# Optimization experiments

Measured on AMD Instinct MI355X. Metric: run time of the kernel, lower is better.

Reference implementation:

```python
import jax, jax.numpy as jnp
import numpy as np

EMBED = 256
HEADS = 8
HDIM = 32
FF = 1024
EPS = 1e-6
EVERY = 8        # stock_attn_every
LAST_DENSE = 16  # stock_attn_last_dense
B, N, T = 2, 256, 256


def rmsnorm(x, w):
    return x * jax.lax.rsqrt(jnp.mean(x * x, axis=-1, keepdims=True) + EPS) * w


def mha(x, Wq, Wk, Wv, Wo, mask=None):
    # x: (B, S, D); mask: (B, S) bool key-padding mask (True = keep)
    b, s, _ = x.shape
    q = (x @ Wq).reshape(b, s, HEADS, HDIM)
    k = (x @ Wk).reshape(b, s, HEADS, HDIM)
    v = (x @ Wv).reshape(b, s, HEADS, HDIM)
    scores = jnp.einsum('bqhd,bkhd->bhqk', q, k) * (HDIM ** -0.5)
    if mask is not None:
        scores = jnp.where(mask[:, None, None, :], scores, jnp.asarray(-1e9, scores.dtype))
    attn = jax.nn.softmax(scores, axis=-1)
    out = jnp.einsum('bhqk,bkhd->bqhd', attn, v).reshape(b, s, HEADS * HDIM)
    return out @ Wo


def active_t(t):
    # static index set: sparse strided steps + last dense window
    lds = max(0, t - LAST_DENSE)
    idx = sorted(set(list(range(0, lds, max(1, EVERY))) + list(range(lds, t))))
    return jnp.asarray(idx, dtype=jnp.int32)


def setup_inputs() -> dict:
    key = jax.random.key(0)
    ks = jax.random.split(key, 16)
    p = lambda k, shape: (jax.random.normal(k, shape, dtype=jnp.float32) * 0.02)
    inp = {
        'h': jax.random.normal(ks[0], (B, N, T, EMBED), dtype=jnp.float32),
        'stock_mask': jnp.ones((B, N), dtype=jnp.int32),
        'norm_t_w': jnp.ones((EMBED,), dtype=jnp.float32),
        'norm_s_w': jnp.ones((EMBED,), dtype=jnp.float32),
        'norm_ff_w': jnp.ones((EMBED,), dtype=jnp.float32),
        'Wq_t': p(ks[1], (EMBED, HEADS * HDIM)),
        'Wk_t': p(ks[2], (EMBED, HEADS * HDIM)),
        'Wv_t': p(ks[3], (EMBED, HEADS * HDIM)),
        'Wo_t': p(ks[4], (HEADS * HDIM, EMBED)),
        'Wq_s': p(ks[5], (EMBED, HEADS * HDIM)),
        'Wk_s': p(ks[6], (EMBED, HEADS * HDIM)),
        'Wv_s': p(ks[7], (EMBED, HEADS * HDIM)),
        'Wo_s': p(ks[8], (HEADS * HDIM, EMBED)),
        'W1': p(ks[9], (EMBED, FF)),
        'b1': jnp.zeros((FF,), dtype=jnp.float32),
        'W2': p(ks[10], (FF, EMBED)),
        'b2': jnp.zeros((EMBED,), dtype=jnp.float32),
    }
    return inp


def reference(h, stock_mask, norm_t_w, norm_s_w, norm_ff_w,
              Wq_t, Wk_t, Wv_t, Wo_t, Wq_s, Wk_s, Wv_s, Wo_s,
              W1, b1, W2, b2):
    b, n, t, d = h.shape
    # --- time attention (per stock, dense over T) ---
    h_t = rmsnorm(h.reshape(b * n, t, d), norm_t_w)
    h = h + mha(h_t, Wq_t, Wk_t, Wv_t, Wo_t).reshape(b, n, t, d)
    # --- sparse-T gather -> stock attention -> scatter back ---
    active = active_t(t)
    tp = active.shape[0]
    h_s = h[:, :, active, :].transpose(0, 2, 1, 3).reshape(b * tp, n, d)
    m = jnp.broadcast_to(stock_mask.astype(bool)[:, None, :], (b, tp, n)).reshape(b * tp, n)
    h_s = mha(rmsnorm(h_s, norm_s_w), Wq_s, Wk_s, Wv_s, Wo_s, mask=m)
    h = h.at[:, :, active, :].add(h_s.reshape(b, tp, n, d).transpose(0, 2, 1, 3))
    # --- FFN ---
    x = rmsnorm(h, norm_ff_w)
    return h + (jax.nn.gelu(x @ W1 + b1) @ W2 + b2)
```

## Files before the change

kernel.cpp:

```cpp
#include <hip/hip_runtime.h>
#include <hip/hip_bf16.h>

typedef __attribute__((ext_vector_type(8))) short short8;
typedef __attribute__((ext_vector_type(4))) float f32x4;

#define TP 46

#define SBAR() asm volatile("s_barrier" ::: "memory")
#define VMCNT4() asm volatile("s_waitcnt vmcnt(4)" ::: "memory")
#define VMCNT0() asm volatile("s_waitcnt vmcnt(0)" ::: "memory")

__device__ __forceinline__ unsigned short f2bf(float f) {
  unsigned int u = __float_as_uint(f);
  u = (u + 0x7fff + ((u >> 16) & 1)) >> 16;
  return (unsigned short)u;
}
__device__ __forceinline__ unsigned short f2bf_fast(float f) {
  return (unsigned short)((__float_as_uint(f) + 0x8000u) >> 16);
}
__device__ __forceinline__ float bf2f(short u) {
  return __uint_as_float((unsigned)(unsigned short)u << 16);
}
__device__ __forceinline__ float fast_rcp(float x) {
#if __has_builtin(__builtin_amdgcn_rcpf)
  return __builtin_amdgcn_rcpf(x);
#else
  return 1.0f / x;
#endif
}
__device__ __forceinline__ float fast_rsq(float x) {
#if __has_builtin(__builtin_amdgcn_rsqf)
  return __builtin_amdgcn_rsqf(x);
#else
  return rsqrtf(x);
#endif
}

__device__ __forceinline__ int act_t(int j) { return j < 30 ? (j << 3) : (210 + j); }

__device__ __forceinline__ void load_lds16(const unsigned short* g, unsigned short* lds_base) {
#if __has_builtin(__builtin_amdgcn_global_load_lds)
  __builtin_amdgcn_global_load_lds(
      (const __attribute__((address_space(1))) unsigned int*)(unsigned long long)g,
      (__attribute__((address_space(3))) unsigned int*)(unsigned int)(unsigned long long)lds_base,
      16, 0, 0);
#else
  int lane = threadIdx.x & 63;
  *(short8*)(lds_base + lane * 8) = *(const short8*)g;
#endif
}

__global__ __launch_bounds__(256) void convw_kernel(
    const float* __restrict__ wq_t, const float* __restrict__ wk_t,
    const float* __restrict__ wv_t, const float* __restrict__ wo_t,
    const float* __restrict__ wq_s, const float* __restrict__ wk_s,
    const float* __restrict__ wv_s, const float* __restrict__ wo_s,
    const float* __restrict__ w1, const float* __restrict__ w2,
    unsigned short* __restrict__ pool) {
  int idx = blockIdx.x * 256 + threadIdx.x;
  float v;
  if (idx < 524288) {
    int tile = idx >> 12, local = idx & 4095;
    int ks = local >> 9, q = local & 511;
    int l = q >> 3, e = q & 7;
    int lr = l & 15, lg = l >> 4;
    int ct = tile & 15, grp = tile >> 4;
    const float* s = (grp == 0) ? wq_t : (grp == 1) ? wk_t : (grp == 2) ? wv_t :
                     (grp == 3) ? wo_t : (grp == 4) ? wq_s : (grp == 5) ? wk_s :
                     (grp == 6) ? wv_s : wo_s;
    v = s[(size_t)(ks * 32 + lg * 8 + e) * 256 + ct * 16 + lr];
  } else if (idx < 786432) {
    int local = idx - 524288;
    int e = local & 7, t = local >> 3;
    int lane = t & 63, ks = (t >> 6) & 7, ct = (t >> 9) & 1, fc = t >> 10;
    int lr = lane & 15, lg = lane >> 4;
    v = w1[(size_t)(ks * 32 + lg * 8 + e) * 1024 + fc * 32 + ct * 16 + lr];
  } else {
    int local = idx - 786432;
    int e2 = local & 7, t = local >> 3;
    int lane = t & 63, ct2 = (t >> 6) & 15, fc = t >> 10;
    int lr = lane & 15, lg = lane >> 4;
    v = w2[(size_t)(fc * 32 + lg * 8 + e2) * 256 + ct2 * 16 + lr];
  }
  pool[idx] = f2bf(v);
}

template<int GATHER>
__global__ __launch_bounds__(256) void qkv_kernel(
    const float* __restrict__ src, const float* __restrict__ nw,
    const unsigned short* __restrict__ WF,
    unsigned short* __restrict__ qb, unsigned short* __restrict__ kb,
    unsigned short* __restrict__ vb, int row_base) {
  __shared__ __align__(16) unsigned short Wbuf[2][8192];
  int tid = threadIdx.x, wv = tid >> 6, lane = tid & 63, lr = lane & 15, lg = lane >> 4;
  int row0 = blockIdx.x * 128 + wv * 32;
  short8 afrag[2][8];
  #pragma unroll
  for (int rt = 0; rt < 2; ++rt) {
    int lrow = row0 + rt * 16 + lr;
    const float* rp;
    if (GATHER) {
      int gr = row_base + lrow;
      int b = gr / 11776; int rem = gr - b * 11776;
      int j = rem >> 8, n = rem & 255;
      rp = src + (((size_t)((b << 8) + n) << 8) + act_t(j)) * 256;
    } else {
      rp = src + (size_t)lrow * 256;
    }
    float4 x[16];
    #pragma unroll
    for (int ks = 0; ks < 8; ++ks) {
      x[ks * 2]     = *(const float4*)(rp + ks * 32 + lg * 8);
      x[ks * 2 + 1] = *(const float4*)(rp + ks * 32 + lg * 8 + 4);
    }
    float ss = 0.f;
    #pragma unroll
    for (int i = 0; i < 16; ++i)
      ss += x[i].x * x[i].x + x[i].y * x[i].y + x[i].z * x[i].z + x[i].w * x[i].w;
    ss += __shfl_xor(ss, 16, 64);
    ss += __shfl_xor(ss, 32, 64);
    float sc = fast_rsq(ss * 0.00390625f + 1e-6f);
    #pragma unroll
    for (int ks = 0; ks < 8; ++ks) {
      float4 w0 = *(const float4*)(nw + ks * 32 + lg * 8);
      float4 w1_ = *(const float4*)(nw + ks * 32 + lg * 8 + 4);
      short8 af;
      af[0] = (short)f2bf_fast(x[ks * 2].x * sc * w0.x);
      af[1] = (short)f2bf_fast(x[ks * 2].y * sc * w0.y);
      af[2] = (short)f2bf_fast(x[ks * 2].z * sc * w0.z);
      af[3] = (short)f2bf_fast(x[ks * 2].w * sc * w0.w);
      af[4] = (short)f2bf_fast(x[ks * 2 + 1].x * sc * w1_.x);
      af[5] = (short)f2bf_fast(x[ks * 2 + 1].y * sc * w1_.y);
      af[6] = (short)f2bf_fast(x[ks * 2 + 1].z * sc * w1_.z);
      af[7] = (short)f2bf_fast(x[ks * 2 + 1].w * sc * w1_.w);
      afrag[rt][ks] = af;
    }
  }
  #pragma unroll
  for (int i = 0; i < 4; ++i) {
    int s = wv * 4 + i;
    load_lds16(WF + (size_t)s * 512 + lane * 8, &Wbuf[0][s * 512]);
  }
  f32x4 zero = {0.f, 0.f, 0.f, 0.f};
  for (int r = 0; r < 24; ++r) {
    SBAR();
    if (r < 23) {
      #pragma unroll
      for (int i = 0; i < 4; ++i) {
        int s = wv * 4 + i;
        load_lds16(WF + (size_t)(r + 1) * 8192 + s * 512 + lane * 8,
                   &Wbuf[(r + 1) & 1][s * 512]);
      }
      VMCNT4();
    } else {
      VMCNT0();
    }
    SBAR();
    #pragma unroll
    for (int sub = 0; sub < 2; ++sub) {
      int t = r * 2 + sub;
      const unsigned short* Ws = &Wbuf[r & 1][sub * 4096];
      f32x4 a0 = zero, a1 = zero;
      #pragma unroll
      for (int ks = 0; ks < 8; ++ks) {
        short8 bw = *(const short8*)&Ws[ks * 512 + lane * 8];
        a0 = __builtin_amdgcn_mfma_f32_16x16x32_bf16(bw, afrag[0][ks], a0, 0, 0, 0);
        a1 = __builtin_amdgcn_mfma_f32_16x16x32_bf16(bw, afrag[1][ks], a1, 0, 0, 0);
      }
      int m = t >> 4, ct = t & 15;
      unsigned short* dst = (m == 0) ? qb : (m == 1) ? kb : vb;
      ushort4 p0, p1;
      p0.x = f2bf_fast(a0[0]); p0.y = f2bf_fast(a0[1]);
      p0.z = f2bf_fast(a0[2]); p0.w = f2bf_fast(a0[3]);
      p1.x = f2bf_fast(a1[0]); p1.y = f2bf_fast(a1[1]);
      p1.z = f2bf_fast(a1[2]); p1.w = f2bf_fast(a1[3]);
      *(ushort4*)(dst + (size_t)(row0 + lr) * 256 + ct * 16 + lg * 4) = p0;
      *(ushort4*)(dst + (size_t)(row0 + 16 + lr) * 256 + ct * 16 + lg * 4) = p1;
    }
  }
}

template<int MODE>
__global__ __launch_bounds__(256) void gemm256_kernel(
    const unsigned short* __restrict__ X, const unsigned short* __restrict__ WF,
    const float* __restrict__ resid, float* __restrict__ outf, int row_base) {
  __shared__ __align__(16) unsigned short Wbuf[2][8192];
  int tid = threadIdx.x, wv = tid >> 6, lane = tid & 63, lr = lane & 15, lg = lane >> 4;
  int row0 = blockIdx.x * 128 + wv * 32;
  short8 afrag[2][8];
  size_t rb[2];
  #pragma unroll
  for (int rt = 0; rt < 2; ++rt) {
    int row = row0 + rt * 16 + lr;
    #pragma unroll
    for (int ks = 0; ks < 8; ++ks)
      afrag[rt][ks] = *(const short8*)(X + (size_t)row * 256 + ks * 32 + lg * 8);
    if (MODE == 1) {
      rb[rt] = (size_t)row * 256;
    } else {
      int gr = row_base + row;
      int b = gr / 11776; int rem = gr - b * 11776;
      int j = rem >> 8, n = rem & 255;
      rb[rt] = (((size_t)((b << 8) + n) << 8) + act_t(j)) * 256;
    }
  }
  #pragma unroll
  for (int i = 0; i < 4; ++i) {
    int s = wv * 4 + i;
    load_lds16(WF + (size_t)s * 512 + lane * 8, &Wbuf[0][s * 512]);
  }
  f32x4 zero = {0.f, 0.f, 0.f, 0.f};
  for (int r = 0; r < 8; ++r) {
    __syncthreads();
    if (r < 7) {
      #pragma unroll
      for (int i = 0; i < 4; ++i) {
        int s = wv * 4 + i;
        load_lds16(WF + (size_t)(r + 1) * 8192 + s * 512 + lane * 8,
                   &Wbuf[(r + 1) & 1][s * 512]);
      }
    }
    __syncthreads();
    #pragma unroll
    for (int sub = 0; sub < 2; ++sub) {
      int t = r * 2 + sub;
      const unsigned short* Ws = &Wbuf[r & 1][sub * 4096];
      f32x4 a0 = zero, a1 = zero;
      #pragma unroll
      for (int ks = 0; ks < 8; ++ks) {
        short8 bw = *(const short8*)&Ws[ks * 512 + lane * 8];
        a0 = __builtin_amdgcn_mfma_f32_16x16x32_bf16(bw, afrag[0][ks], a0, 0, 0, 0);
        a1 = __builtin_amdgcn_mfma_f32_16x16x32_bf16(bw, afrag[1][ks], a1, 0, 0, 0);
      }
      int col = t * 16 + lg * 4;
      if (MODE == 1) {
        float4 r0 = *(const float4*)(resid + rb[0] + col);
        float4 r1 = *(const float4*)(resid + rb[1] + col);
        float4 o0, o1;
        o0.x = r0.x + a0[0]; o0.y = r0.y + a0[1]; o0.z = r0.z + a0[2]; o0.w = r0.w + a0[3];
        o1.x = r1.x + a1[0]; o1.y = r1.y + a1[1]; o1.z = r1.z + a1[2]; o1.w = r1.w + a1[3];
        *(float4*)(outf + rb[0] + col) = o0;
        *(float4*)(outf + rb[1] + col) = o1;
      } else {
        float4 c0 = *(const float4*)(outf + rb[0] + col);
        float4 c1 = *(const float4*)(outf + rb[1] + col);
        c0.x += a0[0]; c0.y += a0[1]; c0.z += a0[2]; c0.w += a0[3];
        c1.x += a1[0]; c1.y += a1[1]; c1.z += a1[2]; c1.w += a1[3];
        *(float4*)(outf + rb[0] + col) = c0;
        *(float4*)(outf + rb[1] + col) = c1;
      }
    }
  }
}

template<int MASKED>
__global__ __launch_bounds__(256) void attn_kernel(
    const unsigned short* __restrict__ Q, const unsigned short* __restrict__ K,
    const unsigned short* __restrict__ V, unsigned short* __restrict__ O,
    const int* __restrict__ mask, int seq_base) {
  __shared__ unsigned short Ksh[256][40];
  __shared__ unsigned short Vtsh[32][264];
  __shared__ unsigned short Psh[4][16][264];
  int head = blockIdx.x, seq = blockIdx.y;
  int hc = head * 32;
  size_t sb = (size_t)seq * 65536;
  int tid = threadIdx.x;
  {
    int c = tid & 3, rbase = tid >> 2;
    #pragma unroll
    for (int i = 0; i < 4; ++i) {
      int r = rbase + i * 64;
      *(short8*)&Ksh[r][c * 8] = *(const short8*)(K + sb + (size_t)r * 256 + hc + c * 8);
      short8 vv = *(const short8*)(V + sb + (size_t)r * 256 + hc + c * 8);
      #pragma unroll
      for (int e = 0; e < 8; ++e) Vtsh[c * 8 + e][r] = (unsigned short)vv[e];
    }
  }
  __syncthreads();
  int wv = tid >> 6, lane = tid & 63, lr = lane & 15, lg = lane >> 4;
  const float scale = 0.17677669529663687f;
  int mb = 0;
  if (MASKED) mb = (seq_base + seq) / TP;
  f32x4 zero = {0.f, 0.f, 0.f, 0.f};
  for (int rt = 0; rt < 4; ++rt) {
    int row0 = wv * 64 + rt * 16;
    short8 aq = *(const short8*)(Q + sb + (size_t)(row0 + lr) * 256 + hc + lg * 8);
    f32x4 s[16];
    #pragma unroll
    for (int ct = 0; ct < 16; ++ct) {
      short8 kb = *(const short8*)&Ksh[ct * 16 + lr][lg * 8];
      s[ct] = __builtin_amdgcn_mfma_f32_16x16x32_bf16(kb, aq, zero, 0, 0, 0);
    }
    #pragma unroll
    for (int ct = 0; ct < 16; ++ct) {
      if (MASKED) {
        const int4 m4 = *(const int4*)(mask + mb * 256 + ct * 16 + lg * 4);
        s[ct][0] = m4.x ? s[ct][0] * scale : -1e9f;
        s[ct][1] = m4.y ? s[ct][1] * scale : -1e9f;
        s[ct][2] = m4.z ? s[ct][2] * scale : -1e9f;
        s[ct][3] = m4.w ? s[ct][3] * scale : -1e9f;
      } else {
        #pragma unroll
        for (int r = 0; r < 4; ++r) s[ct][r] *= scale;
      }
    }
    float mx = -3e38f;
    #pragma unroll
    for (int ct = 0; ct < 16; ++ct)
      #pragma unroll
      for (int r = 0; r < 4; ++r) mx = fmaxf(mx, s[ct][r]);
    mx = fmaxf(mx, __shfl_xor(mx, 16, 64));
    mx = fmaxf(mx, __shfl_xor(mx, 32, 64));
    float sum = 0.f;
    #pragma unroll
    for (int ct = 0; ct < 16; ++ct)
      #pragma unroll
      for (int r = 0; r < 4; ++r) {
        float p = __expf(s[ct][r] - mx);
        s[ct][r] = p; sum += p;
      }
    sum += __shfl_xor(sum, 16, 64);
    sum += __shfl_xor(sum, 32, 64);
    float inv = fast_rcp(sum);
    #pragma unroll
    for (int ct = 0; ct < 16; ++ct) {
      ushort4 pk;
      pk.x = f2bf_fast(s[ct][0] * inv); pk.y = f2bf_fast(s[ct][1] * inv);
      pk.z = f2bf_fast(s[ct][2] * inv); pk.w = f2bf_fast(s[ct][3] * inv);
      *(ushort4*)&Psh[wv][lr][ct * 16 + lg * 4] = pk;
    }
    f32x4 o[2] = {zero, zero};
    #pragma unroll
    for (int ks = 0; ks < 8; ++ks) {
      short8 pa = *(const short8*)&Psh[wv][lr][ks * 32 + lg * 8];
      #pragma unroll
      for (int c2 = 0; c2 < 2; ++c2) {
        short8 vbf = *(const short8*)&Vtsh[c2 * 16 + lr][ks * 32 + lg * 8];
        o[c2] = __builtin_amdgcn_mfma_f32_16x16x32_bf16(vbf, pa, o[c2], 0, 0, 0);
      }
    }
    #pragma unroll
    for (int c2 = 0; c2 < 2; ++c2) {
      ushort4 ok;
      ok.x = f2bf_fast(o[c2][0]); ok.y = f2bf_fast(o[c2][1]);
      ok.z = f2bf_fast(o[c2][2]); ok.w = f2bf_fast(o[c2][3]);
      *(ushort4*)(O + sb + (size_t)(row0 + lr) * 256 + hc + c2 * 16 + lg * 4) = ok;
    }
  }
}

__global__ __launch_bounds__(256, 4) void ffn_kernel(
    float* __restrict__ hio, const float* __restrict__ nw,
    const unsigned short* __restrict__ W1F, const unsigned short* __restrict__ W2F,
    const float* __restrict__ b1, const float* __restrict__ b2) {
  __shared__ __align__(16) unsigned short Wbuf[16384];
  __shared__ __align__(16) unsigned short Psh[4][16][36];
  int tid = threadIdx.x;
  int wv = tid >> 6, lane = tid & 63, lr = lane & 15, lg = lane >> 4;
  int wrow = blockIdx.x * 64 + wv * 16;
  const float* rp = hio + (size_t)(wrow + lr) * 256;
  short8 xfrag[8];
  float ss = 0.f;
  #pragma unroll
  for (int ks = 0; ks < 8; ++ks) {
    float4 a = *(const float4*)(rp + ks * 32 + lg * 8);
    float4 b = *(const float4*)(rp + ks * 32 + lg * 8 + 4);
    ss += a.x * a.x + a.y * a.y + a.z * a.z + a.w * a.w;
    ss += b.x * b.x + b.y * b.y + b.z * b.z + b.w * b.w;
    short8 xf;
    xf[0] = (short)f2bf_fast(a.x); xf[1] = (short)f2bf_fast(a.y);
    xf[2] = (short)f2bf_fast(a.z); xf[3] = (short)f2bf_fast(a.w);
    xf[4] = (short)f2bf_fast(b.x); xf[5] = (short)f2bf_fast(b.y);
    xf[6] = (short)f2bf_fast(b.z); xf[7] = (short)f2bf_fast(b.w);
    xfrag[ks] = xf;
  }
  ss += __shfl_xor(ss, 16, 64);
  ss += __shfl_xor(ss, 32, 64);
  float sc = fast_rsq(ss * 0.00390625f + 1e-6f);
  #pragma unroll
  for (int ks = 0; ks < 8; ++ks) {
    float4 wa = *(const float4*)(nw + ks * 32 + lg * 8);
    float4 wb = *(const float4*)(nw + ks * 32 + lg * 8 + 4);
    short8 xf = xfrag[ks], af;
    af[0] = (short)f2bf_fast(bf2f(xf[0]) * sc * wa.x);
    af[1] = (short)f2bf_fast(bf2f(xf[1]) * sc * wa.y);
    af[2] = (short)f2bf_fast(bf2f(xf[2]) * sc * wa.z);
    af[3] = (short)f2bf_fast(bf2f(xf[3]) * sc * wa.w);
    af[4] = (short)f2bf_fast(bf2f(xf[4]) * sc * wb.x);
    af[5] = (short)f2bf_fast(bf2f(xf[5]) * sc * wb.y);
    af[6] = (short)f2bf_fast(bf2f(xf[6]) * sc * wb.z);
    af[7] = (short)f2bf_fast(bf2f(xf[7]) * sc * wb.w);
    xfrag[ks] = af;
  }
  f32x4 zero = {0.f, 0.f, 0.f, 0.f};
  f32x4 oacc[16];
  #pragma unroll
  for (int ct = 0; ct < 16; ++ct) oacc[ct] = zero;
  for (int fc = 0; fc < 32; ++fc) {
    __syncthreads();
    #pragma unroll
    for (int i = 0; i < 8; ++i) {
      int s = wv * 8 + i;
      const unsigned short* srcp = (s < 16) ? (W1F + (size_t)fc * 8192 + s * 512)
                                            : (W2F + (size_t)fc * 8192 + (s - 16) * 512);
      load_lds16(srcp + lane * 8, &Wbuf[s * 512]);
    }
    __syncthreads();
    const unsigned short* W1s = &Wbuf[0];
    const unsigned short* W2s = &Wbuf[8192];
    f32x4 hacc[2];
    hacc[0] = zero; hacc[1] = zero;
    #pragma unroll
    for (int ks = 0; ks < 8; ++ks) {
      #pragma unroll
      for (int ct = 0; ct < 2; ++ct) {
        short8 w1f = *(const short8*)&W1s[(ct * 8 + ks) * 512 + lane * 8];
        hacc[ct] = __builtin_amdgcn_mfma_f32_16x16x32_bf16(w1f, xfrag[ks], hacc[ct], 0, 0, 0);
      }
    }
    #pragma unroll
    for (int ct = 0; ct < 2; ++ct) {
      float4 bb = *(const float4*)(b1 + fc * 32 + ct * 16 + lg * 4);
      ushort4 pk;
      float hv = hacc[ct][0] + bb.x;
      pk.x = f2bf_fast(hv * fast_rcp(1.0f + __expf(-1.5957691216057308f * fmaf(0.044715f * hv, hv * hv, hv))));
      hv = hacc[ct][1] + bb.y;
      pk.y = f2bf_fast(hv * fast_rcp(1.0f + __expf(-1.5957691216057308f * fmaf(0.044715f * hv, hv * hv, hv))));
      hv = hacc[ct][2] + bb.z;
      pk.z = f2bf_fast(hv * fast_rcp(1.0f + __expf(-1.5957691216057308f * fmaf(0.044715f * hv, hv * hv, hv))));
      hv = hacc[ct][3] + bb.w;
      pk.w = f2bf_fast(hv * fast_rcp(1.0f + __expf(-1.5957691216057308f * fmaf(0.044715f * hv, hv * hv, hv))));
      *(ushort4*)&Psh[wv][lr][ct * 16 + lg * 4] = pk;
    }
    short8 pa = *(const short8*)&Psh[wv][lr][lg * 8];
    #pragma unroll
    for (int ct2 = 0; ct2 < 16; ++ct2) {
      short8 bw2 = *(const short8*)&W2s[ct2 * 512 + lane * 8];
      oacc[ct2] = __builtin_amdgcn_mfma_f32_16x16x32_bf16(bw2, pa, oacc[ct2], 0, 0, 0);
    }
  }
  size_t rbase = (size_t)(wrow + lr) * 256;
  #pragma unroll
  for (int ct2 = 0; ct2 < 16; ++ct2) {
    int col = ct2 * 16 + lg * 4;
    float4 bb2 = *(const float4*)(b2 + col);
    float4 cur = *(const float4*)(hio + rbase + col);
    cur.x += oacc[ct2][0] + bb2.x;
    cur.y += oacc[ct2][1] + bb2.y;
    cur.z += oacc[ct2][2] + bb2.z;
    cur.w += oacc[ct2][3] + bb2.w;
    *(float4*)(hio + rbase + col) = cur;
  }
}

extern "C" void kernel_launch(void* const* d_in, const int* in_sizes, int n_in,
                              void* d_out, int out_size, void* d_ws, size_t ws_size,
                              hipStream_t stream) {
  (void)in_sizes; (void)n_in; (void)out_size;
  const float* h   = (const float*)d_in[0];
  const int* smask = (const int*)d_in[1];
  const float* ntw = (const float*)d_in[2];
  const float* nsw = (const float*)d_in[3];
  const float* nfw = (const float*)d_in[4];
  const float* wq_t = (const float*)d_in[5];
  const float* wk_t = (const float*)d_in[6];
  const float* wv_t = (const float*)d_in[7];
  const float* wo_t = (const float*)d_in[8];
  const float* wq_s = (const float*)d_in[9];
  const float* wk_s = (const float*)d_in[10];
  const float* wv_s = (const float*)d_in[11];
  const float* wo_s = (const float*)d_in[12];
  const float* w1  = (const float*)d_in[13];
  const float* b1  = (const float*)d_in[14];
  const float* w2  = (const float*)d_in[15];
  const float* b2  = (const float*)d_in[16];
  float* out = (float*)d_out;
  unsigned short* pool = (unsigned short*)d_ws;

  unsigned short* WQKVtF = pool;
  unsigned short* WOtF   = pool + 196608;
  unsigned short* WQKVsF = pool + 262144;
  unsigned short* WOsF   = pool + 458752;
  unsigned short* W1F    = pool + 524288;
  unsigned short* W2F    = pool + 786432;

  size_t wbytes = 1048576ull * 2;
  size_t avail = (ws_size > wbytes) ? (ws_size - wbytes) : 0;
  long long scl = (long long)(avail / 524288ull);
  int SC = scl < 1 ? 1 : (scl > 512 ? 512 : (int)scl);
  unsigned short* xnorm = pool + 1048576;
  unsigned short* qb = xnorm + (size_t)SC * 65536;
  unsigned short* kb = qb + (size_t)SC * 65536;
  unsigned short* vb = kb + (size_t)SC * 65536;

  convw_kernel<<<4096, 256, 0, stream>>>(wq_t, wk_t, wv_t, wo_t, wq_s, wk_s, wv_s,
                                         wo_s, w1, w2, pool);

  for (int s0 = 0; s0 < 512; s0 += SC) {
    int ns = (512 - s0 < SC) ? (512 - s0) : SC;
    int rows = ns * 256;
    qkv_kernel<0><<<rows / 128, 256, 0, stream>>>(h + (size_t)s0 * 65536, ntw, WQKVtF,
                                                  qb, kb, vb, 0);
    attn_kernel<0><<<dim3(8, ns), 256, 0, stream>>>(qb, kb, vb, xnorm, nullptr, 0);
    gemm256_kernel<1><<<rows / 128, 256, 0, stream>>>(xnorm, WOtF,
        h + (size_t)s0 * 65536, out + (size_t)s0 * 65536, 0);
  }

  int SC2 = SC < 92 ? SC : 92;
  for (int s0 = 0; s0 < 92; s0 += SC2) {
    int ns = (92 - s0 < SC2) ? (92 - s0) : SC2;
    int rows = ns * 256;
    qkv_kernel<1><<<rows / 128, 256, 0, stream>>>(out, nsw, WQKVsF, qb, kb, vb, s0 * 256);
    attn_kernel<1><<<dim3(8, ns), 256, 0, stream>>>(qb, kb, vb, xnorm, smask, s0);
    gemm256_kernel<2><<<rows / 128, 256, 0, stream>>>(xnorm, WOsF, nullptr, out, s0 * 256);
  }

  ffn_kernel<<<2048, 256, 0, stream>>>(out, nfw, W1F, W2F, b1, b2);
}
```

Measured before the change: 702.3 us.

## Write V transposed from QKV kernel and read K/V directly from global in attention

The QKV projection now emits V in a transposed per-sequence layout by swapping MFMA operands for the V tiles, so the attention kernel no longer needs to transpose V through shared memory. The attention kernel also drops its K and V shared-memory staging and barrier, loading MFMA fragments straight from global memory and relying on cache reuse across the four waves. This removes LDS traffic, the scalar transpose stores and a sync. In exchange it adds redundant global/L2 reads per wave and more scattered writes of V in the QKV epilogue.

```diff
diff --git a/kernel.cpp b/kernel.cpp
--- a/kernel.cpp
+++ b/kernel.cpp
@@ -90,7 +90,7 @@
     const float* __restrict__ src, const float* __restrict__ nw,
     const unsigned short* __restrict__ WF,
     unsigned short* __restrict__ qb, unsigned short* __restrict__ kb,
-    unsigned short* __restrict__ vb, int row_base) {
+    unsigned short* __restrict__ vt, int row_base) {
   __shared__ __align__(16) unsigned short Wbuf[2][8192];
   int tid = threadIdx.x, wv = tid >> 6, lane = tid & 63, lr = lane & 15, lg = lane >> 4;
   int row0 = blockIdx.x * 128 + wv * 32;
@@ -142,6 +142,8 @@
     load_lds16(WF + (size_t)s * 512 + lane * 8, &Wbuf[0][s * 512]);
   }
   f32x4 zero = {0.f, 0.f, 0.f, 0.f};
+  int seq_local = row0 >> 8;
+  int keybase = row0 & 255;
   for (int r = 0; r < 24; ++r) {
     SBAR();
     if (r < 23) {
@@ -160,22 +162,39 @@
     for (int sub = 0; sub < 2; ++sub) {
       int t = r * 2 + sub;
       const unsigned short* Ws = &Wbuf[r & 1][sub * 4096];
+      int m = t >> 4, ct = t & 15;
       f32x4 a0 = zero, a1 = zero;
-      #pragma unroll
-      for (int ks = 0; ks < 8; ++ks) {
-        short8 bw = *(const short8*)&Ws[ks * 512 + lane * 8];
-        a0 = __builtin_amdgcn_mfma_f32_16x16x32_bf16(bw, afrag[0][ks], a0, 0, 0, 0);
-        a1 = __builtin_amdgcn_mfma_f32_16x16x32_bf16(bw, afrag[1][ks], a1, 0, 0, 0);
-      }
-      int m = t >> 4, ct = t & 15;
-      unsigned short* dst = (m == 0) ? qb : (m == 1) ? kb : vb;
-      ushort4 p0, p1;
-      p0.x = f2bf_fast(a0[0]); p0.y = f2bf_fast(a0[1]);
-      p0.z = f2bf_fast(a0[2]); p0.w = f2bf_fast(a0[3]);
-      p1.x = f2bf_fast(a1[0]); p1.y = f2bf_fast(a1[1]);
-      p1.z = f2bf_fast(a1[2]); p1.w = f2bf_fast(a1[3]);
-      *(ushort4*)(dst + (size_t)(row0 + lr) * 256 + ct * 16 + lg * 4) = p0;
-      *(ushort4*)(dst + (size_t)(row0 + 16 + lr) * 256 + ct * 16 + lg * 4) = p1;
+      if (m < 2) {
+        #pragma unroll
+        for (int ks = 0; ks < 8; ++ks) {
+          short8 bw = *(const short8*)&Ws[ks * 512 + lane * 8];
+          a0 = __builtin_amdgcn_mfma_f32_16x16x32_bf16(bw, afrag[0][ks], a0, 0, 0, 0);
+          a1 = __builtin_amdgcn_mfma_f32_16x16x32_bf16(bw, afrag[1][ks], a1, 0, 0, 0);
+        }
+        unsigned short* dst = (m == 0) ? qb : kb;
+        ushort4 p0, p1;
+        p0.x = f2bf_fast(a0[0]); p0.y = f2bf_fast(a0[1]);
+        p0.z = f2bf_fast(a0[2]); p0.w = f2bf_fast(a0[3]);
+        p1.x = f2bf_fast(a1[0]); p1.y = f2bf_fast(a1[1]);
+        p1.z = f2bf_fast(a1[2]); p1.w = f2bf_fast(a1[3]);
+        *(ushort4*)(dst + (size_t)(row0 + lr) * 256 + ct * 16 + lg * 4) = p0;
+        *(ushort4*)(dst + (size_t)(row0 + 16 + lr) * 256 + ct * 16 + lg * 4) = p1;
+      } else {
+        #pragma unroll
+        for (int ks = 0; ks < 8; ++ks) {
+          short8 bw = *(const short8*)&Ws[ks * 512 + lane * 8];
+          a0 = __builtin_amdgcn_mfma_f32_16x16x32_bf16(afrag[0][ks], bw, a0, 0, 0, 0);
+          a1 = __builtin_amdgcn_mfma_f32_16x16x32_bf16(afrag[1][ks], bw, a1, 0, 0, 0);
+        }
+        ushort4 p0, p1;
+        p0.x = f2bf_fast(a0[0]); p0.y = f2bf_fast(a0[1]);
+        p0.z = f2bf_fast(a0[2]); p0.w = f2bf_fast(a0[3]);
+        p1.x = f2bf_fast(a1[0]); p1.y = f2bf_fast(a1[1]);
+        p1.z = f2bf_fast(a1[2]); p1.w = f2bf_fast(a1[3]);
+        size_t cbase = ((size_t)(seq_local * 256 + ct * 16 + lr)) * 256;
+        *(ushort4*)(vt + cbase + keybase + lg * 4) = p0;
+        *(ushort4*)(vt + cbase + keybase + 16 + lg * 4) = p1;
+      }
     }
   }
 }
@@ -256,27 +275,13 @@
 template<int MASKED>
 __global__ __launch_bounds__(256) void attn_kernel(
     const unsigned short* __restrict__ Q, const unsigned short* __restrict__ K,
-    const unsigned short* __restrict__ V, unsigned short* __restrict__ O,
+    const unsigned short* __restrict__ VT, unsigned short* __restrict__ O,
     const int* __restrict__ mask, int seq_base) {
-  __shared__ unsigned short Ksh[256][40];
-  __shared__ unsigned short Vtsh[32][264];
   __shared__ unsigned short Psh[4][16][264];
   int head = blockIdx.x, seq = blockIdx.y;
   int hc = head * 32;
   size_t sb = (size_t)seq * 65536;
   int tid = threadIdx.x;
-  {
-    int c = tid & 3, rbase = tid >> 2;
-    #pragma unroll
-    for (int i = 0; i < 4; ++i) {
-      int r = rbase + i * 64;
-      *(short8*)&Ksh[r][c * 8] = *(const short8*)(K + sb + (size_t)r * 256 + hc + c * 8);
-      short8 vv = *(const short8*)(V + sb + (size_t)r * 256 + hc + c * 8);
-      #pragma unroll
-      for (int e = 0; e < 8; ++e) Vtsh[c * 8 + e][r] = (unsigned short)vv[e];
-    }
-  }
-  __syncthreads();
   int wv = tid >> 6, lane = tid & 63, lr = lane & 15, lg = lane >> 4;
   const float scale = 0.17677669529663687f;
   int mb = 0;
@@ -288,7 +293,7 @@
     f32x4 s[16];
     #pragma unroll
     for (int ct = 0; ct < 16; ++ct) {
-      short8 kb = *(const short8*)&Ksh[ct * 16 + lr][lg * 8];
+      short8 kb = *(const short8*)(K + sb + (size_t)(ct * 16 + lr) * 256 + hc + lg * 8);
       s[ct] = __builtin_amdgcn_mfma_f32_16x16x32_bf16(kb, aq, zero, 0, 0, 0);
     }
     #pragma unroll
@@ -335,7 +340,8 @@
       short8 pa = *(const short8*)&Psh[wv][lr][ks * 32 + lg * 8];
       #pragma unroll
       for (int c2 = 0; c2 < 2; ++c2) {
-        short8 vbf = *(const short8*)&Vtsh[c2 * 16 + lr][ks * 32 + lg * 8];
+        short8 vbf = *(const short8*)(VT +
+            ((size_t)(seq * 256 + hc + c2 * 16 + lr)) * 256 + ks * 32 + lg * 8);
         o[c2] = __builtin_amdgcn_mfma_f32_16x16x32_bf16(vbf, pa, o[c2], 0, 0, 0);
       }
     }
@@ -491,7 +497,7 @@
   unsigned short* xnorm = pool + 1048576;
   unsigned short* qb = xnorm + (size_t)SC * 65536;
   unsigned short* kb = qb + (size_t)SC * 65536;
-  unsigned short* vb = kb + (size_t)SC * 65536;
+  unsigned short* vt = kb + (size_t)SC * 65536;
 
   convw_kernel<<<4096, 256, 0, stream>>>(wq_t, wk_t, wv_t, wo_t, wq_s, wk_s, wv_s,
                                          wo_s, w1, w2, pool);
@@ -500,8 +506,8 @@
     int ns = (512 - s0 < SC) ? (512 - s0) : SC;
     int rows = ns * 256;
     qkv_kernel<0><<<rows / 128, 256, 0, stream>>>(h + (size_t)s0 * 65536, ntw, WQKVtF,
-                                                  qb, kb, vb, 0);
-    attn_kernel<0><<<dim3(8, ns), 256, 0, stream>>>(qb, kb, vb, xnorm, nullptr, 0);
+                                                  qb, kb, vt, 0);
+    attn_kernel<0><<<dim3(8, ns), 256, 0, stream>>>(qb, kb, vt, xnorm, nullptr, 0);
     gemm256_kernel<1><<<rows / 128, 256, 0, stream>>>(xnorm, WOtF,
         h + (size_t)s0 * 65536, out + (size_t)s0 * 65536, 0);
   }
@@ -510,8 +516,8 @@
   for (int s0 = 0; s0 < 92; s0 += SC2) {
     int ns = (92 - s0 < SC2) ? (92 - s0) : SC2;
     int rows = ns * 256;
-    qkv_kernel<1><<<rows / 128, 256, 0, stream>>>(out, nsw, WQKVsF, qb, kb, vb, s0 * 256);
-    attn_kernel<1><<<dim3(8, ns), 256, 0, stream>>>(qb, kb, vb, xnorm, smask, s0);
+    qkv_kernel<1><<<rows / 128, 256, 0, stream>>>(out, nsw, WQKVsF, qb, kb, vt, s0 * 256);
+    attn_kernel<1><<<dim3(8, ns), 256, 0, stream>>>(qb, kb, vt, xnorm, smask, s0);
     gemm256_kernel<2><<<rows / 128, 256, 0, stream>>>(xnorm, WOsF, nullptr, out, s0 * 256);
   }
 
```

Result: slower. 758.8 us, median of 2 (+8.0%).
